# Optimization experiments

Hardware: AMD Instinct MI355X
Metric: run time of the kernel (lower is better)

The kernel has to match this reference:

```python
import jax, jax.numpy as jnp
import numpy as np
import math

NUM_HEADS = 16
HEAD_DIM = 64


def _apply_rope(x, sin2, cos2):
    # x: [B,H,S,D]; sin2/cos2: [1,1,S,D] interleaved-duplicated sin/cos
    x_even = x[..., ::2]
    x_odd = x[..., 1::2]
    rot = jnp.stack([-x_odd, x_even], axis=-1).reshape(x.shape)
    return x * cos2 + rot * sin2


def setup_inputs() -> dict:
    key = jax.random.key(0)
    k1, k2, k3, k4 = jax.random.split(key, 4)
    B, S, D = 2, 2048, 1024
    hidden_states = jax.random.normal(k1, (B, S, D), dtype=jnp.float32)
    # RoFormer-style sinusoidal_pos: first half sin, second half cos
    half = HEAD_DIM // 2
    inv_freq = 1.0 / (10000.0 ** (np.arange(0, half, dtype=np.float32) / half))
    t = np.arange(S, dtype=np.float32)
    ang = np.einsum('s,d->sd', t, inv_freq)  # [S, half]
    sinusoidal_pos = jnp.asarray(
        np.concatenate([np.sin(ang), np.cos(ang)], axis=-1)[None, None]
    )  # [1,1,S,HEAD_DIM]
    attention_mask = jnp.zeros((B, 1, 1, S), dtype=jnp.float32)
    scale = 0.02
    Wq = jax.random.normal(k2, (D, D), dtype=jnp.float32) * scale
    Wk = jax.random.normal(k3, (D, D), dtype=jnp.float32) * scale
    Wv = jax.random.normal(k4, (D, D), dtype=jnp.float32) * scale
    return {
        'hidden_states': hidden_states,
        'sinusoidal_pos': sinusoidal_pos,
        'attention_mask': attention_mask,
        'Wq': Wq,
        'Wk': Wk,
        'Wv': Wv,
    }


def reference(hidden_states, sinusoidal_pos, attention_mask, Wq, Wk, Wv):
    B, S, D = hidden_states.shape
    H, Dh = NUM_HEADS, HEAD_DIM

    def split_heads(x):  # [B,S,D] -> [B,H,S,Dh]
        return x.reshape(B, S, H, Dh).transpose(0, 2, 1, 3)

    q = split_heads(hidden_states @ Wq.T)
    k = split_heads(hidden_states @ Wk.T)
    v = split_heads(hidden_states @ Wv.T)

    # sinusoidal_pos: [1,1,S,Dh]; chunk -> sin, cos halves, then interleave-duplicate
    sin, cos = jnp.split(sinusoidal_pos, 2, axis=-1)
    sin2 = jnp.repeat(sin, 2, axis=-1)
    cos2 = jnp.repeat(cos, 2, axis=-1)
    q = _apply_rope(q, sin2, cos2)
    k = _apply_rope(k, sin2, cos2)

    scores = jnp.einsum('bhqd,bhkd->bhqk', q, k) / math.sqrt(Dh)
    scores = scores + attention_mask  # additive mask broadcasts over heads/query
    probs = jax.nn.softmax(scores, axis=-1)
    ctx = jnp.einsum('bhqk,bhkd->bhqd', probs, v)
    ctx = ctx.transpose(0, 2, 1, 3).reshape(B, S, D)
    return ctx
```

## Files before the change

kernel.cpp:

```cpp
#include <hip/hip_runtime.h>
#include <math.h>

#define B_  2
#define S_  2048
#define D_  1024
#define H_  16
#define DH  64
#define M_  (B_*S_)
#define QKSZ 4194304

typedef __attribute__((ext_vector_type(4)))  float  f32x4;
typedef __attribute__((ext_vector_type(16))) float  f32x16;
typedef __attribute__((ext_vector_type(8)))  short  short8;
typedef __attribute__((ext_vector_type(8)))  unsigned short ushort8;
typedef __attribute__((ext_vector_type(4)))  unsigned short us4;

static __device__ __forceinline__ unsigned short f2bf(float x) {
    union { float f; unsigned int u; } v; v.f = x;
    unsigned int u = v.u;
    u += 0x7fffu + ((u >> 16) & 1u);
    return (unsigned short)(u >> 16);
}

typedef __attribute__((address_space(3))) void       lds_void;
typedef const __attribute__((address_space(1))) void gbl_void;

static __device__ __forceinline__ void gload_lds16(const unsigned short* g,
                                                   unsigned short* l) {
    __builtin_amdgcn_global_load_lds((gbl_void*)g, (lds_void*)l, 16, 0, 0);
}

__global__ __launch_bounds__(256) void cvt_all(
    const float* __restrict__ hid, const float* __restrict__ Wq,
    const float* __restrict__ Wk,  const float* __restrict__ Wv,
    unsigned short* __restrict__ hb, unsigned short* __restrict__ wb)
{
    const size_t i = ((size_t)blockIdx.x * 256 + threadIdx.x) * 8;
    const float* s; unsigned short* d;
    if (i < 4194304) { s = hid + i; d = hb + i; }
    else {
        size_t j = i - 4194304;
        const float* w = (j < 1048576) ? Wq : (j < 2097152) ? Wk : Wv;
        s = w + (j & 1048575);
        d = wb + j;
    }
    float4 a = *(const float4*)s, b = *(const float4*)(s + 4);
    ushort8 o;
    o[0] = f2bf(a.x); o[1] = f2bf(a.y); o[2] = f2bf(a.z); o[3] = f2bf(a.w);
    o[4] = f2bf(b.x); o[5] = f2bf(b.y); o[6] = f2bf(b.z); o[7] = f2bf(b.w);
    *(ushort8*)d = o;
}

__global__ __launch_bounds__(256) void qkv_gemm(
    const unsigned short* __restrict__ hb,
    const unsigned short* __restrict__ wb,
    const float* __restrict__ sp,
    unsigned short* __restrict__ qk_ws,
    unsigned short* __restrict__ vt_ws)
{
    __shared__ unsigned short As[128 * 32];
    __shared__ unsigned short Bs[128 * 32];

    const int tid    = threadIdx.x;
    const int tile_m = (blockIdx.x & 31) * 128;
    const int tile_n = (blockIdx.x >> 5) * 128;

    const int w  = tid >> 6, lane = tid & 63;
    const int wr = w >> 1,  wc = w & 1;
    const int g  = lane >> 4, c16 = lane & 15;
    const int lr = lane >> 2;
    const int lc = (lane & 3) * 8;

    const size_t arow = (size_t)(tile_m + w * 16 + lr) * 1024 + lc;
    const size_t brow = (size_t)(tile_n + w * 16 + lr) * 1024 + lc;
    unsigned short* lA0 = &As[(w * 16) * 32];
    unsigned short* lA1 = &As[(w * 16 + 64) * 32];
    unsigned short* lB0 = &Bs[(w * 16) * 32];
    unsigned short* lB1 = &Bs[(w * 16 + 64) * 32];

    f32x4 acc[4][4];
    #pragma unroll
    for (int i = 0; i < 4; ++i)
        #pragma unroll
        for (int j = 0; j < 4; ++j)
            acc[i][j][0] = acc[i][j][1] = acc[i][j][2] = acc[i][j][3] = 0.f;

    for (int k0 = 0; k0 < 1024; k0 += 32) {
        gload_lds16(hb + arow + k0,             lA0);
        gload_lds16(hb + arow + 64 * 1024 + k0, lA1);
        gload_lds16(wb + brow + k0,             lB0);
        gload_lds16(wb + brow + 64 * 1024 + k0, lB1);
        __syncthreads();

        short8 af[4], bf[4];
        #pragma unroll
        for (int i = 0; i < 4; ++i)
            af[i] = *(const short8*)&As[(wr * 64 + i * 16 + c16) * 32 + g * 8];
        #pragma unroll
        for (int j = 0; j < 4; ++j)
            bf[j] = *(const short8*)&Bs[(wc * 64 + j * 16 + c16) * 32 + g * 8];
        __builtin_amdgcn_s_setprio(1);
        #pragma unroll
        for (int i = 0; i < 4; ++i)
            #pragma unroll
            for (int j = 0; j < 4; ++j)
                acc[i][j] = __builtin_amdgcn_mfma_f32_16x16x32_bf16(
                    af[i], bf[j], acc[i][j], 0, 0, 0);
        __builtin_amdgcn_s_setprio(0);
        __syncthreads();
    }

    if (tile_n < 2048) {
        const int isK = (tile_n >= 1024) ? 1 : 0;
        unsigned short* qkb = qk_ws + (size_t)isK * QKSZ;
        const int head = ((tile_n - (isK ? 1024 : 0)) + wc * 64) >> 6;
        #pragma unroll
        for (int j = 0; j < 4; ++j) {
            const int dh = j * 16 + c16;
            const int p  = dh >> 1;
            const int odd = dh & 1;
            #pragma unroll
            for (int i = 0; i < 4; ++i) {
                #pragma unroll
                for (int r = 0; r < 4; ++r) {
                    const int m = tile_m + wr * 64 + i * 16 + 4 * g + r;
                    const int b = m >> 11, s = m & 2047;
                    float v    = acc[i][j][r];
                    float part = __shfl_xor(v, 1);
                    float sv = sp[s * 64 + p];
                    float cv = sp[s * 64 + 32 + p];
                    float o  = odd ? (v * cv + part * sv) : (v * cv - part * sv);
                    qkb[((size_t)(b * H_ + head) * S_ + s) * DH + dh] = f2bf(o);
                }
            }
        }
    } else {
        const int head = (tile_n - 2048 + wc * 64) >> 6;
        #pragma unroll
        for (int j = 0; j < 4; ++j) {
            const int dh = j * 16 + c16;
            #pragma unroll
            for (int i = 0; i < 4; ++i) {
                const int m0 = tile_m + wr * 64 + i * 16 + 4 * g;
                const int b = m0 >> 11, s0 = m0 & 2047;
                us4 o;
                o[0] = f2bf(acc[i][j][0]); o[1] = f2bf(acc[i][j][1]);
                o[2] = f2bf(acc[i][j][2]); o[3] = f2bf(acc[i][j][3]);
                *(us4*)&vt_ws[((size_t)(b * H_ + head) * DH + dh) * S_ + s0] = o;
            }
        }
    }
}

__global__ __launch_bounds__(256) void qkv_proj(
    const float* __restrict__ hid,
    const float* __restrict__ sp,
    const float* __restrict__ Wq,
    const float* __restrict__ Wk,
    const float* __restrict__ Wv,
    unsigned short* __restrict__ qk_ws,
    unsigned short* __restrict__ vt_ws)
{
    __shared__ unsigned short As[128 * 32];
    __shared__ unsigned short Bs[128 * 32];

    const int tid    = threadIdx.x;
    const int tile_m = (blockIdx.x & 31) * 128;
    const int tile_n = (blockIdx.x >> 5) * 128;

    const float* W; int nloc;
    if (tile_n < 1024)      { W = Wq; nloc = tile_n; }
    else if (tile_n < 2048) { W = Wk; nloc = tile_n - 1024; }
    else                    { W = Wv; nloc = tile_n - 2048; }

    const int w    = tid >> 6, lane = tid & 63;
    const int wr   = w >> 1,  wc   = w & 1;
    const int g    = lane >> 4, c16 = lane & 15;
    const int srow = tid >> 3;
    const int scol = (tid & 7) * 4;

    f32x4 acc[4][4];
    #pragma unroll
    for (int i = 0; i < 4; ++i)
        #pragma unroll
        for (int j = 0; j < 4; ++j)
            acc[i][j][0] = acc[i][j][1] = acc[i][j][2] = acc[i][j][3] = 0.f;

    for (int k0 = 0; k0 < 1024; k0 += 32) {
        #pragma unroll
        for (int p = 0; p < 4; ++p) {
            const int row = p * 32 + srow;
            float4 a = *(const float4*)&hid[(size_t)(tile_m + row) * 1024 + k0 + scol];
            float4 b = *(const float4*)&W  [(size_t)(nloc   + row) * 1024 + k0 + scol];
            us4 ap, bp;
            ap[0] = f2bf(a.x); ap[1] = f2bf(a.y); ap[2] = f2bf(a.z); ap[3] = f2bf(a.w);
            bp[0] = f2bf(b.x); bp[1] = f2bf(b.y); bp[2] = f2bf(b.z); bp[3] = f2bf(b.w);
            *(us4*)&As[p * 1024 + tid * 4] = ap;
            *(us4*)&Bs[p * 1024 + tid * 4] = bp;
        }
        __syncthreads();

        short8 af[4], bf[4];
        #pragma unroll
        for (int i = 0; i < 4; ++i)
            af[i] = *(const short8*)&As[(wr * 64 + i * 16 + c16) * 32 + g * 8];
        #pragma unroll
        for (int j = 0; j < 4; ++j)
            bf[j] = *(const short8*)&Bs[(wc * 64 + j * 16 + c16) * 32 + g * 8];
        #pragma unroll
        for (int i = 0; i < 4; ++i)
            #pragma unroll
            for (int j = 0; j < 4; ++j)
                acc[i][j] = __builtin_amdgcn_mfma_f32_16x16x32_bf16(
                    af[i], bf[j], acc[i][j], 0, 0, 0);
        __syncthreads();
    }

    if (tile_n < 2048) {
        const int isK = (tile_n >= 1024) ? 1 : 0;
        unsigned short* qkb = qk_ws + (size_t)isK * QKSZ;
        const int head = ((tile_n - (isK ? 1024 : 0)) + wc * 64) >> 6;
        #pragma unroll
        for (int j = 0; j < 4; ++j) {
            const int dh = j * 16 + c16;
            const int p  = dh >> 1;
            const int odd = dh & 1;
            #pragma unroll
            for (int i = 0; i < 4; ++i) {
                #pragma unroll
                for (int r = 0; r < 4; ++r) {
                    const int m = tile_m + wr * 64 + i * 16 + 4 * g + r;
                    const int b = m >> 11, s = m & 2047;
                    float v    = acc[i][j][r];
                    float part = __shfl_xor(v, 1);
                    float sv = sp[s * 64 + p];
                    float cv = sp[s * 64 + 32 + p];
                    float o  = odd ? (v * cv + part * sv) : (v * cv - part * sv);
                    qkb[((size_t)(b * H_ + head) * S_ + s) * DH + dh] = f2bf(o);
                }
            }
        }
    } else {
        const int head = (tile_n - 2048 + wc * 64) >> 6;
        #pragma unroll
        for (int j = 0; j < 4; ++j) {
            const int dh = j * 16 + c16;
            #pragma unroll
            for (int i = 0; i < 4; ++i) {
                const int m0 = tile_m + wr * 64 + i * 16 + 4 * g;
                const int b = m0 >> 11, s0 = m0 & 2047;
                us4 o;
                o[0] = f2bf(acc[i][j][0]); o[1] = f2bf(acc[i][j][1]);
                o[2] = f2bf(acc[i][j][2]); o[3] = f2bf(acc[i][j][3]);
                *(us4*)&vt_ws[((size_t)(b * H_ + head) * DH + dh) * S_ + s0] = o;
            }
        }
    }
}

__global__ __launch_bounds__(256, 2) void attn_fwd(
    const unsigned short* __restrict__ qk_ws,
    const unsigned short* __restrict__ vt_ws,
    const float* __restrict__ maskp,
    float* __restrict__ out)
{
    __shared__ unsigned short K_lds[2][64 * 64];
    __shared__ unsigned short V_lds[2][64 * 64];

    const int tid  = threadIdx.x;
    const int w    = tid >> 6, lane = tid & 63;
    const int hi   = lane >> 5, c32 = lane & 31;
    const int qt   = blockIdx.x & 15;
    const int bh   = blockIdx.x >> 4;
    const int b    = bh >> 4, h = bh & 15;

    const unsigned short* qp = qk_ws + (size_t)bh * (S_ * DH);
    const unsigned short* kp = qk_ws + QKSZ + (size_t)bh * (S_ * DH);
    const unsigned short* vp = vt_ws + (size_t)bh * (DH * S_);
    const float* mp = maskp + b * S_;

    const int q = qt * 128 + w * 32 + c32;

    short8 qf[4];
    #pragma unroll
    for (int ks = 0; ks < 4; ++ks)
        qf[ks] = *(const short8*)&qp[(size_t)q * DH + ks * 16 + 8 * hi];

    f32x16 ctx[2];
    #pragma unroll
    for (int d = 0; d < 2; ++d)
        #pragma unroll
        for (int r = 0; r < 16; ++r) ctx[d][r] = 0.f;
    float mrow = -1e30f, lsum = 0.f;

    ushort8 rk[2], rv[2];
    const int su0 = tid, su1 = tid + 256;

    auto LOADT = [&](int t) {
        const int kv = t * 64;
        {
            int row = su0 >> 3, c = (su0 & 7) * 8;
            rk[0] = *(const ushort8*)&kp[(size_t)(kv + row) * DH + c];
            rv[0] = *(const ushort8*)&vp[(size_t)row * S_ + kv + c];
        }
        {
            int row = su1 >> 3, c = (su1 & 7) * 8;
            rk[1] = *(const ushort8*)&kp[(size_t)(kv + row) * DH + c];
            rv[1] = *(const ushort8*)&vp[(size_t)row * S_ + kv + c];
        }
    };
    auto WRITET = [&](int buf) {
        {
            int row = su0 >> 3, c = (su0 & 7) * 16;
            int off = (row * 128 + c) ^ ((row & 7) << 4);
            *(ushort8*)((char*)&K_lds[buf][0] + off) = rk[0];
            *(ushort8*)((char*)&V_lds[buf][0] + off) = rv[0];
        }
        {
            int row = su1 >> 3, c = (su1 & 7) * 16;
            int off = (row * 128 + c) ^ ((row & 7) << 4);
            *(ushort8*)((char*)&K_lds[buf][0] + off) = rk[1];
            *(ushort8*)((char*)&V_lds[buf][0] + off) = rv[1];
        }
    };

    LOADT(0); WRITET(0); LOADT(1);
    __syncthreads();

    const int NT = S_ / 64;
    for (int t = 0; t < NT; ++t) {
        const int cur = t & 1;
        const int kv  = t * 64;
        const char* Kb = (const char*)&K_lds[cur][0];
        const char* Vb = (const char*)&V_lds[cur][0];

        f32x16 sa0, sa1;
        #pragma unroll
        for (int r = 0; r < 16; ++r) { sa0[r] = 0.f; sa1[r] = 0.f; }
        __builtin_amdgcn_s_setprio(1);
        #pragma unroll
        for (int ks = 0; ks < 4; ++ks) {
            const int colb = ks * 32 + hi * 16;
            short8 kf0 = *(const short8*)(Kb + ((c32 * 128 + colb) ^ ((c32 & 7) << 4)));
            short8 kf1 = *(const short8*)(Kb + (((32 + c32) * 128 + colb) ^ ((c32 & 7) << 4)));
            sa0 = __builtin_amdgcn_mfma_f32_32x32x16_bf16(kf0, qf[ks], sa0, 0, 0, 0);
            sa1 = __builtin_amdgcn_mfma_f32_32x32x16_bf16(kf1, qf[ks], sa1, 0, 0, 0);
        }
        __builtin_amdgcn_s_setprio(0);

        float sc0[16], sc1[16];
        #pragma unroll
        for (int r = 0; r < 16; ++r) {
            const int koff = (r & 3) + 8 * (r >> 2) + 4 * hi;
            sc0[r] = sa0[r] * 0.125f + mp[kv + koff];
            sc1[r] = sa1[r] * 0.125f + mp[kv + 32 + koff];
        }

        float pm = sc0[0];
        #pragma unroll
        for (int r = 1; r < 16; ++r) pm = fmaxf(pm, sc0[r]);
        #pragma unroll
        for (int r = 0; r < 16; ++r) pm = fmaxf(pm, sc1[r]);
        pm = fmaxf(pm, __shfl_xor(pm, 32));

        if (!__all(pm - mrow <= 8.0f)) {
            const float mnew = fmaxf(mrow, pm);
            const float fac  = __expf(mrow - mnew);
            mrow = mnew;
            lsum *= fac;
            #pragma unroll
            for (int d = 0; d < 2; ++d)
                #pragma unroll
                for (int r = 0; r < 16; ++r) ctx[d][r] *= fac;
        }

        float p0[16], p1[16];
        float ps = 0.f;
        #pragma unroll
        for (int r = 0; r < 16; ++r) { p0[r] = __expf(sc0[r] - mrow); ps += p0[r]; }
        #pragma unroll
        for (int r = 0; r < 16; ++r) { p1[r] = __expf(sc1[r] - mrow); ps += p1[r]; }
        lsum += ps;

        short8 pf[4];
        #pragma unroll
        for (int ks4 = 0; ks4 < 4; ++ks4) {
            const float* pp = (ks4 < 2) ? p0 : p1;
            const int k8 = (ks4 & 1) * 8;
            unsigned int a0 = ((unsigned int)f2bf(pp[k8 + 1]) << 16) | f2bf(pp[k8 + 0]);
            unsigned int a1 = ((unsigned int)f2bf(pp[k8 + 3]) << 16) | f2bf(pp[k8 + 2]);
            unsigned int b0 = ((unsigned int)f2bf(pp[k8 + 5]) << 16) | f2bf(pp[k8 + 4]);
            unsigned int b1 = ((unsigned int)f2bf(pp[k8 + 7]) << 16) | f2bf(pp[k8 + 6]);
            unsigned int ax0 = (unsigned int)__shfl_xor((int)a0, 32);
            unsigned int ax1 = (unsigned int)__shfl_xor((int)a1, 32);
            unsigned int bx0 = (unsigned int)__shfl_xor((int)b0, 32);
            unsigned int bx1 = (unsigned int)__shfl_xor((int)b1, 32);
            union { unsigned int u[4]; short8 v; } fr;
            fr.u[0] = hi ? bx0 : a0;
            fr.u[1] = hi ? bx1 : a1;
            fr.u[2] = hi ? b0  : ax0;
            fr.u[3] = hi ? b1  : ax1;
            pf[ks4] = fr.v;
        }

        if (t + 1 < NT) {
            __syncthreads();
            WRITET(cur ^ 1);
            if (t + 2 < NT) LOADT(t + 2);
        }

        __builtin_amdgcn_s_setprio(1);
        #pragma unroll
        for (int ks4 = 0; ks4 < 4; ++ks4) {
            const int colb = ks4 * 32 + hi * 16;
            short8 vf0 = *(const short8*)(Vb + ((c32 * 128 + colb) ^ ((c32 & 7) << 4)));
            short8 vf1 = *(const short8*)(Vb + (((32 + c32) * 128 + colb) ^ ((c32 & 7) << 4)));
            ctx[0] = __builtin_amdgcn_mfma_f32_32x32x16_bf16(vf0, pf[ks4], ctx[0], 0, 0, 0);
            ctx[1] = __builtin_amdgcn_mfma_f32_32x32x16_bf16(vf1, pf[ks4], ctx[1], 0, 0, 0);
        }
        __builtin_amdgcn_s_setprio(0);

        if (t + 1 < NT) __syncthreads();
    }

    const float inv = 1.0f / (lsum + __shfl_xor(lsum, 32));

    float* ob = out + ((size_t)(b * S_ + q) * D_) + h * DH;
    #pragma unroll
    for (int d = 0; d < 2; ++d)
        #pragma unroll
        for (int q4 = 0; q4 < 4; ++q4) {
            f32x4 st;
            st[0] = ctx[d][q4 * 4 + 0] * inv;
            st[1] = ctx[d][q4 * 4 + 1] * inv;
            st[2] = ctx[d][q4 * 4 + 2] * inv;
            st[3] = ctx[d][q4 * 4 + 3] * inv;
            *(f32x4*)&ob[d * 32 + 8 * q4 + 4 * hi] = st;
        }
}

extern "C" void kernel_launch(void* const* d_in, const int* in_sizes, int n_in,
                              void* d_out, int out_size, void* d_ws, size_t ws_size,
                              hipStream_t stream) {
    (void)in_sizes; (void)n_in; (void)out_size;
    const float* hid  = (const float*)d_in[0];
    const float* sp   = (const float*)d_in[1];
    const float* mask = (const float*)d_in[2];
    const float* Wq   = (const float*)d_in[3];
    const float* Wk   = (const float*)d_in[4];
    const float* Wv   = (const float*)d_in[5];
    float* out = (float*)d_out;

    unsigned short* qk_ws = (unsigned short*)d_ws;
    unsigned short* vt_ws = qk_ws + 2 * (size_t)QKSZ;
    unsigned short* hb    = vt_ws + (size_t)QKSZ;
    unsigned short* wb    = hb + 4194304;

    const size_t NEED = 39845888;
    if (ws_size >= NEED) {
        cvt_all<<<dim3(3584), dim3(256), 0, stream>>>(hid, Wq, Wk, Wv, hb, wb);
        qkv_gemm<<<dim3(32 * 24), dim3(256), 0, stream>>>(hb, wb, sp, qk_ws, vt_ws);
    } else {
        qkv_proj<<<dim3(32 * 24), dim3(256), 0, stream>>>(hid, sp, Wq, Wk, Wv, qk_ws, vt_ws);
    }
    attn_fwd<<<dim3(32 * 16), dim3(256), 0, stream>>>(qk_ws, vt_ws, mask, out);
}
```

Baseline: 197.2 us.

## Widen GEMM K-tile with swizzled LDS, fold softmax scale into Q, use exp2

The QKV GEMM now stages a 64-wide K slice per iteration into XOR-swizzled LDS, which halves the barrier count and is meant to cut LDS bank conflicts. The attention kernel pre-scales Q by log2(e)/sqrt(d) in the GEMM epilogue and uses raw v_exp_f32 (exp2), which drops the per-score multiply. It also caches the mask in LDS pre-multiplied by log2(e), uses packed bf16 conversion for P, and changes the rescale threshold and max reduction. The risks are higher LDS use, which may lower occupancy, and small numerical differences from scaling Q before bf16 rounding.

```diff
diff --git a/kernel.cpp b/kernel.cpp
--- a/kernel.cpp
+++ b/kernel.cpp
@@ -1,4 +1,5 @@
 #include <hip/hip_runtime.h>
+#include <hip/hip_bf16.h>
 #include <math.h>
 
 #define B_  2
@@ -6,7 +7,6 @@
 #define D_  1024
 #define H_  16
 #define DH  64
-#define M_  (B_*S_)
 #define QKSZ 4194304
 
 typedef __attribute__((ext_vector_type(4)))  float  f32x4;
@@ -15,11 +15,26 @@
 typedef __attribute__((ext_vector_type(8)))  unsigned short ushort8;
 typedef __attribute__((ext_vector_type(4)))  unsigned short us4;
 
+#define LOG2E 1.44269504f
+#define QSCL  0.18033688f
+
 static __device__ __forceinline__ unsigned short f2bf(float x) {
     union { float f; unsigned int u; } v; v.f = x;
     unsigned int u = v.u;
     u += 0x7fffu + ((u >> 16) & 1u);
     return (unsigned short)(u >> 16);
+}
+
+static __device__ __forceinline__ unsigned int pk2(float lo, float hi) {
+    union { __hip_bfloat162 b; unsigned int u; } c;
+    c.b = __float22bfloat162_rn(float2{lo, hi});
+    return c.u;
+}
+
+static __device__ __forceinline__ float exp2a(float x) {
+    float r;
+    asm("v_exp_f32 %0, %1" : "=v"(r) : "v"(x));
+    return r;
 }
 
 typedef __attribute__((address_space(3))) void       lds_void;
@@ -58,8 +73,8 @@
     unsigned short* __restrict__ qk_ws,
     unsigned short* __restrict__ vt_ws)
 {
-    __shared__ unsigned short As[128 * 32];
-    __shared__ unsigned short Bs[128 * 32];
+    __shared__ unsigned short As[128 * 64];
+    __shared__ unsigned short Bs[128 * 64];
 
     const int tid    = threadIdx.x;
     const int tile_m = (blockIdx.x & 31) * 128;
@@ -68,15 +83,11 @@
     const int w  = tid >> 6, lane = tid & 63;
     const int wr = w >> 1,  wc = w & 1;
     const int g  = lane >> 4, c16 = lane & 15;
-    const int lr = lane >> 2;
-    const int lc = (lane & 3) * 8;
-
-    const size_t arow = (size_t)(tile_m + w * 16 + lr) * 1024 + lc;
-    const size_t brow = (size_t)(tile_n + w * 16 + lr) * 1024 + lc;
-    unsigned short* lA0 = &As[(w * 16) * 32];
-    unsigned short* lA1 = &As[(w * 16 + 64) * 32];
-    unsigned short* lB0 = &Bs[(w * 16) * 32];
-    unsigned short* lB1 = &Bs[(w * 16 + 64) * 32];
+
+    const int rg = lane >> 3;
+    const int cg = (lane & 7) ^ rg;
+    const size_t a_base = (size_t)(tile_m + w * 8 + rg) * 1024 + cg * 8;
+    const size_t b_base = (size_t)(tile_n + w * 8 + rg) * 1024 + cg * 8;
 
     f32x4 acc[4][4];
     #pragma unroll
@@ -85,33 +96,42 @@
         for (int j = 0; j < 4; ++j)
             acc[i][j][0] = acc[i][j][1] = acc[i][j][2] = acc[i][j][3] = 0.f;
 
-    for (int k0 = 0; k0 < 1024; k0 += 32) {
-        gload_lds16(hb + arow + k0,             lA0);
-        gload_lds16(hb + arow + 64 * 1024 + k0, lA1);
-        gload_lds16(wb + brow + k0,             lB0);
-        gload_lds16(wb + brow + 64 * 1024 + k0, lB1);
+    for (int k0 = 0; k0 < 1024; k0 += 64) {
+        #pragma unroll
+        for (int p = 0; p < 4; ++p) {
+            gload_lds16(hb + a_base + (size_t)p * 32768 + k0, &As[(p * 32 + w * 8) * 64]);
+            gload_lds16(wb + b_base + (size_t)p * 32768 + k0, &Bs[(p * 32 + w * 8) * 64]);
+        }
         __syncthreads();
 
-        short8 af[4], bf[4];
-        #pragma unroll
-        for (int i = 0; i < 4; ++i)
-            af[i] = *(const short8*)&As[(wr * 64 + i * 16 + c16) * 32 + g * 8];
-        #pragma unroll
-        for (int j = 0; j < 4; ++j)
-            bf[j] = *(const short8*)&Bs[(wc * 64 + j * 16 + c16) * 32 + g * 8];
-        __builtin_amdgcn_s_setprio(1);
-        #pragma unroll
-        for (int i = 0; i < 4; ++i)
-            #pragma unroll
-            for (int j = 0; j < 4; ++j)
-                acc[i][j] = __builtin_amdgcn_mfma_f32_16x16x32_bf16(
-                    af[i], bf[j], acc[i][j], 0, 0, 0);
-        __builtin_amdgcn_s_setprio(0);
+        #pragma unroll
+        for (int kk = 0; kk < 2; ++kk) {
+            short8 af[4], bf[4];
+            #pragma unroll
+            for (int i = 0; i < 4; ++i) {
+                const int row = wr * 64 + i * 16 + c16;
+                af[i] = *(const short8*)&As[row * 64 + (((kk << 2) + g) ^ (row & 7)) * 8];
+            }
+            #pragma unroll
+            for (int j = 0; j < 4; ++j) {
+                const int row = wc * 64 + j * 16 + c16;
+                bf[j] = *(const short8*)&Bs[row * 64 + (((kk << 2) + g) ^ (row & 7)) * 8];
+            }
+            __builtin_amdgcn_s_setprio(1);
+            #pragma unroll
+            for (int i = 0; i < 4; ++i)
+                #pragma unroll
+                for (int j = 0; j < 4; ++j)
+                    acc[i][j] = __builtin_amdgcn_mfma_f32_16x16x32_bf16(
+                        af[i], bf[j], acc[i][j], 0, 0, 0);
+            __builtin_amdgcn_s_setprio(0);
+        }
         __syncthreads();
     }
 
     if (tile_n < 2048) {
         const int isK = (tile_n >= 1024) ? 1 : 0;
+        const float qscl = isK ? 1.0f : QSCL;
         unsigned short* qkb = qk_ws + (size_t)isK * QKSZ;
         const int head = ((tile_n - (isK ? 1024 : 0)) + wc * 64) >> 6;
         #pragma unroll
@@ -129,7 +149,7 @@
                     float part = __shfl_xor(v, 1);
                     float sv = sp[s * 64 + p];
                     float cv = sp[s * 64 + 32 + p];
-                    float o  = odd ? (v * cv + part * sv) : (v * cv - part * sv);
+                    float o  = (odd ? (v * cv + part * sv) : (v * cv - part * sv)) * qscl;
                     qkb[((size_t)(b * H_ + head) * S_ + s) * DH + dh] = f2bf(o);
                 }
             }
@@ -150,6 +170,198 @@
             }
         }
     }
+}
+
+__global__ __launch_bounds__(256, 2) void attn_fwd(
+    const unsigned short* __restrict__ qk_ws,
+    const unsigned short* __restrict__ vt_ws,
+    const float* __restrict__ maskp,
+    float* __restrict__ out)
+{
+    __shared__ unsigned short K_lds[2][64 * 64];
+    __shared__ unsigned short V_lds[2][64 * 64];
+    __shared__ float M_lds[2048];
+
+    const int tid  = threadIdx.x;
+    const int w    = tid >> 6, lane = tid & 63;
+    const int hi   = lane >> 5, c32 = lane & 31;
+    const int qt   = blockIdx.x & 15;
+    const int bh   = blockIdx.x >> 4;
+    const int b    = bh >> 4, h = bh & 15;
+
+    const unsigned short* qp = qk_ws + (size_t)bh * (S_ * DH);
+    const unsigned short* kp = qk_ws + QKSZ + (size_t)bh * (S_ * DH);
+    const unsigned short* vp = vt_ws + (size_t)bh * (DH * S_);
+    const float* mp = maskp + b * S_;
+
+    const int q = qt * 128 + w * 32 + c32;
+
+    short8 qf[4];
+    #pragma unroll
+    for (int ks = 0; ks < 4; ++ks)
+        qf[ks] = *(const short8*)&qp[(size_t)q * DH + ks * 16 + 8 * hi];
+
+    f32x16 ctx[2];
+    #pragma unroll
+    for (int d = 0; d < 2; ++d)
+        #pragma unroll
+        for (int r = 0; r < 16; ++r) ctx[d][r] = 0.f;
+    float mrow = -1e30f, lsum = 0.f;
+
+    ushort8 rk[2], rv[2];
+    const int su0 = tid, su1 = tid + 256;
+
+    auto LOADT = [&](int t) {
+        const int kv = t * 64;
+        {
+            int row = su0 >> 3, c = (su0 & 7) * 8;
+            rk[0] = *(const ushort8*)&kp[(size_t)(kv + row) * DH + c];
+            rv[0] = *(const ushort8*)&vp[(size_t)row * S_ + kv + c];
+        }
+        {
+            int row = su1 >> 3, c = (su1 & 7) * 8;
+            rk[1] = *(const ushort8*)&kp[(size_t)(kv + row) * DH + c];
+            rv[1] = *(const ushort8*)&vp[(size_t)row * S_ + kv + c];
+        }
+    };
+    auto WRITET = [&](int buf) {
+        {
+            int row = su0 >> 3, c = (su0 & 7) * 16;
+            int off = (row * 128 + c) ^ ((row & 7) << 4);
+            *(ushort8*)((char*)&K_lds[buf][0] + off) = rk[0];
+            *(ushort8*)((char*)&V_lds[buf][0] + off) = rv[0];
+        }
+        {
+            int row = su1 >> 3, c = (su1 & 7) * 16;
+            int off = (row * 128 + c) ^ ((row & 7) << 4);
+            *(ushort8*)((char*)&K_lds[buf][0] + off) = rk[1];
+            *(ushort8*)((char*)&V_lds[buf][0] + off) = rv[1];
+        }
+    };
+
+    LOADT(0); WRITET(0); LOADT(1);
+    {
+        float4 ma = *(const float4*)&mp[tid * 8];
+        float4 mb2 = *(const float4*)&mp[tid * 8 + 4];
+        M_lds[tid * 8 + 0] = ma.x * LOG2E;  M_lds[tid * 8 + 1] = ma.y * LOG2E;
+        M_lds[tid * 8 + 2] = ma.z * LOG2E;  M_lds[tid * 8 + 3] = ma.w * LOG2E;
+        M_lds[tid * 8 + 4] = mb2.x * LOG2E; M_lds[tid * 8 + 5] = mb2.y * LOG2E;
+        M_lds[tid * 8 + 6] = mb2.z * LOG2E; M_lds[tid * 8 + 7] = mb2.w * LOG2E;
+    }
+    __syncthreads();
+
+    const int NT = S_ / 64;
+    for (int t = 0; t < NT; ++t) {
+        const int cur = t & 1;
+        const int kv  = t * 64;
+        const char* Kb = (const char*)&K_lds[cur][0];
+        const char* Vb = (const char*)&V_lds[cur][0];
+
+        f32x16 sa0, sa1;
+        #pragma unroll
+        for (int r = 0; r < 16; ++r) { sa0[r] = 0.f; sa1[r] = 0.f; }
+        __builtin_amdgcn_s_setprio(1);
+        #pragma unroll
+        for (int ks = 0; ks < 4; ++ks) {
+            const int colb = ks * 32 + hi * 16;
+            short8 kf0 = *(const short8*)(Kb + ((c32 * 128 + colb) ^ ((c32 & 7) << 4)));
+            short8 kf1 = *(const short8*)(Kb + (((32 + c32) * 128 + colb) ^ ((c32 & 7) << 4)));
+            sa0 = __builtin_amdgcn_mfma_f32_32x32x16_bf16(kf0, qf[ks], sa0, 0, 0, 0);
+            sa1 = __builtin_amdgcn_mfma_f32_32x32x16_bf16(kf1, qf[ks], sa1, 0, 0, 0);
+        }
+        __builtin_amdgcn_s_setprio(0);
+
+        float sc0[16], sc1[16];
+        #pragma unroll
+        for (int r = 0; r < 16; ++r) {
+            const int koff = (r & 3) + 8 * (r >> 2) + 4 * hi;
+            sc0[r] = sa0[r] + M_lds[kv + koff];
+            sc1[r] = sa1[r] + M_lds[kv + 32 + koff];
+        }
+
+        float tm[8];
+        #pragma unroll
+        for (int r2 = 0; r2 < 8; ++r2)
+            tm[r2] = fmaxf(fmaxf(sc0[r2 * 2], sc0[r2 * 2 + 1]),
+                           fmaxf(sc1[r2 * 2], sc1[r2 * 2 + 1]));
+        float pm = fmaxf(fmaxf(fmaxf(tm[0], tm[1]), fmaxf(tm[2], tm[3])),
+                         fmaxf(fmaxf(tm[4], tm[5]), fmaxf(tm[6], tm[7])));
+        pm = fmaxf(pm, __shfl_xor(pm, 32));
+
+        if (!__all(pm - mrow <= 11.54f)) {
+            const float mnew = fmaxf(mrow, pm);
+            const float fac  = exp2a(mrow - mnew);
+            mrow = mnew;
+            lsum *= fac;
+            #pragma unroll
+            for (int d = 0; d < 2; ++d)
+                #pragma unroll
+                for (int r = 0; r < 16; ++r) ctx[d][r] *= fac;
+        }
+
+        float p0[16], p1[16];
+        float ps = 0.f;
+        #pragma unroll
+        for (int r = 0; r < 16; ++r) { p0[r] = exp2a(sc0[r] - mrow); ps += p0[r]; }
+        #pragma unroll
+        for (int r = 0; r < 16; ++r) { p1[r] = exp2a(sc1[r] - mrow); ps += p1[r]; }
+        lsum += ps;
+
+        short8 pf[4];
+        #pragma unroll
+        for (int ks4 = 0; ks4 < 4; ++ks4) {
+            const float* pp = (ks4 < 2) ? p0 : p1;
+            const int k8 = (ks4 & 1) * 8;
+            unsigned int a0 = pk2(pp[k8 + 0], pp[k8 + 1]);
+            unsigned int a1 = pk2(pp[k8 + 2], pp[k8 + 3]);
+            unsigned int b0 = pk2(pp[k8 + 4], pp[k8 + 5]);
+            unsigned int b1 = pk2(pp[k8 + 6], pp[k8 + 7]);
+            unsigned int ax0 = (unsigned int)__shfl_xor((int)a0, 32);
+            unsigned int ax1 = (unsigned int)__shfl_xor((int)a1, 32);
+            unsigned int bx0 = (unsigned int)__shfl_xor((int)b0, 32);
+            unsigned int bx1 = (unsigned int)__shfl_xor((int)b1, 32);
+            union { unsigned int u[4]; short8 v; } fr;
+            fr.u[0] = hi ? bx0 : a0;
+            fr.u[1] = hi ? bx1 : a1;
+            fr.u[2] = hi ? b0  : ax0;
+            fr.u[3] = hi ? b1  : ax1;
+            pf[ks4] = fr.v;
+        }
+
+        if (t + 1 < NT) {
+            __syncthreads();
+            WRITET(cur ^ 1);
+            if (t + 2 < NT) LOADT(t + 2);
+        }
+
+        __builtin_amdgcn_s_setprio(1);
+        #pragma unroll
+        for (int ks4 = 0; ks4 < 4; ++ks4) {
+            const int colb = ks4 * 32 + hi * 16;
+            short8 vf0 = *(const short8*)(Vb + ((c32 * 128 + colb) ^ ((c32 & 7) << 4)));
+            short8 vf1 = *(const short8*)(Vb + (((32 + c32) * 128 + colb) ^ ((c32 & 7) << 4)));
+            ctx[0] = __builtin_amdgcn_mfma_f32_32x32x16_bf16(vf0, pf[ks4], ctx[0], 0, 0, 0);
+            ctx[1] = __builtin_amdgcn_mfma_f32_32x32x16_bf16(vf1, pf[ks4], ctx[1], 0, 0, 0);
+        }
+        __builtin_amdgcn_s_setprio(0);
+
+        if (t + 1 < NT) __syncthreads();
+    }
+
+    const float inv = 1.0f / (lsum + __shfl_xor(lsum, 32));
+
+    float* ob = out + ((size_t)(b * S_ + q) * D_) + h * DH;
+    #pragma unroll
+    for (int d = 0; d < 2; ++d)
+        #pragma unroll
+        for (int q4 = 0; q4 < 4; ++q4) {
+            f32x4 st;
+            st[0] = ctx[d][q4 * 4 + 0] * inv;
+            st[1] = ctx[d][q4 * 4 + 1] * inv;
+            st[2] = ctx[d][q4 * 4 + 2] * inv;
+            st[3] = ctx[d][q4 * 4 + 3] * inv;
+            *(f32x4*)&ob[d * 32 + 8 * q4 + 4 * hi] = st;
+        }
 }
 
 __global__ __launch_bounds__(256) void qkv_proj(
@@ -218,6 +430,7 @@
 
     if (tile_n < 2048) {
         const int isK = (tile_n >= 1024) ? 1 : 0;
+        const float qscl = isK ? 1.0f : QSCL;
         unsigned short* qkb = qk_ws + (size_t)isK * QKSZ;
         const int head = ((tile_n - (isK ? 1024 : 0)) + wc * 64) >> 6;
         #pragma unroll
@@ -235,7 +448,7 @@
                     float part = __shfl_xor(v, 1);
                     float sv = sp[s * 64 + p];
                     float cv = sp[s * 64 + 32 + p];
-                    float o  = odd ? (v * cv + part * sv) : (v * cv - part * sv);
+                    float o  = (odd ? (v * cv + part * sv) : (v * cv - part * sv)) * qscl;
                     qkb[((size_t)(b * H_ + head) * S_ + s) * DH + dh] = f2bf(o);
                 }
             }
@@ -256,187 +469,6 @@
             }
         }
     }
-}
-
-__global__ __launch_bounds__(256, 2) void attn_fwd(
-    const unsigned short* __restrict__ qk_ws,
-    const unsigned short* __restrict__ vt_ws,
-    const float* __restrict__ maskp,
-    float* __restrict__ out)
-{
-    __shared__ unsigned short K_lds[2][64 * 64];
-    __shared__ unsigned short V_lds[2][64 * 64];
-
-    const int tid  = threadIdx.x;
-    const int w    = tid >> 6, lane = tid & 63;
-    const int hi   = lane >> 5, c32 = lane & 31;
-    const int qt   = blockIdx.x & 15;
-    const int bh   = blockIdx.x >> 4;
-    const int b    = bh >> 4, h = bh & 15;
-
-    const unsigned short* qp = qk_ws + (size_t)bh * (S_ * DH);
-    const unsigned short* kp = qk_ws + QKSZ + (size_t)bh * (S_ * DH);
-    const unsigned short* vp = vt_ws + (size_t)bh * (DH * S_);
-    const float* mp = maskp + b * S_;
-
-    const int q = qt * 128 + w * 32 + c32;
-
-    short8 qf[4];
-    #pragma unroll
-    for (int ks = 0; ks < 4; ++ks)
-        qf[ks] = *(const short8*)&qp[(size_t)q * DH + ks * 16 + 8 * hi];
-
-    f32x16 ctx[2];
-    #pragma unroll
-    for (int d = 0; d < 2; ++d)
-        #pragma unroll
-        for (int r = 0; r < 16; ++r) ctx[d][r] = 0.f;
-    float mrow = -1e30f, lsum = 0.f;
-
-    ushort8 rk[2], rv[2];
-    const int su0 = tid, su1 = tid + 256;
-
-    auto LOADT = [&](int t) {
-        const int kv = t * 64;
-        {
-            int row = su0 >> 3, c = (su0 & 7) * 8;
-            rk[0] = *(const ushort8*)&kp[(size_t)(kv + row) * DH + c];
-            rv[0] = *(const ushort8*)&vp[(size_t)row * S_ + kv + c];
-        }
-        {
-            int row = su1 >> 3, c = (su1 & 7) * 8;
-            rk[1] = *(const ushort8*)&kp[(size_t)(kv + row) * DH + c];
-            rv[1] = *(const ushort8*)&vp[(size_t)row * S_ + kv + c];
-        }
-    };
-    auto WRITET = [&](int buf) {
-        {
-            int row = su0 >> 3, c = (su0 & 7) * 16;
-            int off = (row * 128 + c) ^ ((row & 7) << 4);
-            *(ushort8*)((char*)&K_lds[buf][0] + off) = rk[0];
-            *(ushort8*)((char*)&V_lds[buf][0] + off) = rv[0];
-        }
-        {
-            int row = su1 >> 3, c = (su1 & 7) * 16;
-            int off = (row * 128 + c) ^ ((row & 7) << 4);
-            *(ushort8*)((char*)&K_lds[buf][0] + off) = rk[1];
-            *(ushort8*)((char*)&V_lds[buf][0] + off) = rv[1];
-        }
-    };
-
-    LOADT(0); WRITET(0); LOADT(1);
-    __syncthreads();
-
-    const int NT = S_ / 64;
-    for (int t = 0; t < NT; ++t) {
-        const int cur = t & 1;
-        const int kv  = t * 64;
-        const char* Kb = (const char*)&K_lds[cur][0];
-        const char* Vb = (const char*)&V_lds[cur][0];
-
-        f32x16 sa0, sa1;
-        #pragma unroll
-        for (int r = 0; r < 16; ++r) { sa0[r] = 0.f; sa1[r] = 0.f; }
-        __builtin_amdgcn_s_setprio(1);
-        #pragma unroll
-        for (int ks = 0; ks < 4; ++ks) {
-            const int colb = ks * 32 + hi * 16;
-            short8 kf0 = *(const short8*)(Kb + ((c32 * 128 + colb) ^ ((c32 & 7) << 4)));
-            short8 kf1 = *(const short8*)(Kb + (((32 + c32) * 128 + colb) ^ ((c32 & 7) << 4)));
-            sa0 = __builtin_amdgcn_mfma_f32_32x32x16_bf16(kf0, qf[ks], sa0, 0, 0, 0);
-            sa1 = __builtin_amdgcn_mfma_f32_32x32x16_bf16(kf1, qf[ks], sa1, 0, 0, 0);
-        }
-        __builtin_amdgcn_s_setprio(0);
-
-        float sc0[16], sc1[16];
-        #pragma unroll
-        for (int r = 0; r < 16; ++r) {
-            const int koff = (r & 3) + 8 * (r >> 2) + 4 * hi;
-            sc0[r] = sa0[r] * 0.125f + mp[kv + koff];
-            sc1[r] = sa1[r] * 0.125f + mp[kv + 32 + koff];
-        }
-
-        float pm = sc0[0];
-        #pragma unroll
-        for (int r = 1; r < 16; ++r) pm = fmaxf(pm, sc0[r]);
-        #pragma unroll
-        for (int r = 0; r < 16; ++r) pm = fmaxf(pm, sc1[r]);
-        pm = fmaxf(pm, __shfl_xor(pm, 32));
-
-        if (!__all(pm - mrow <= 8.0f)) {
-            const float mnew = fmaxf(mrow, pm);
-            const float fac  = __expf(mrow - mnew);
-            mrow = mnew;
-            lsum *= fac;
-            #pragma unroll
-            for (int d = 0; d < 2; ++d)
-                #pragma unroll
-                for (int r = 0; r < 16; ++r) ctx[d][r] *= fac;
-        }
-
-        float p0[16], p1[16];
-        float ps = 0.f;
-        #pragma unroll
-        for (int r = 0; r < 16; ++r) { p0[r] = __expf(sc0[r] - mrow); ps += p0[r]; }
-        #pragma unroll
-        for (int r = 0; r < 16; ++r) { p1[r] = __expf(sc1[r] - mrow); ps += p1[r]; }
-        lsum += ps;
-
-        short8 pf[4];
-        #pragma unroll
-        for (int ks4 = 0; ks4 < 4; ++ks4) {
-            const float* pp = (ks4 < 2) ? p0 : p1;
-            const int k8 = (ks4 & 1) * 8;
-            unsigned int a0 = ((unsigned int)f2bf(pp[k8 + 1]) << 16) | f2bf(pp[k8 + 0]);
-            unsigned int a1 = ((unsigned int)f2bf(pp[k8 + 3]) << 16) | f2bf(pp[k8 + 2]);
-            unsigned int b0 = ((unsigned int)f2bf(pp[k8 + 5]) << 16) | f2bf(pp[k8 + 4]);
-            unsigned int b1 = ((unsigned int)f2bf(pp[k8 + 7]) << 16) | f2bf(pp[k8 + 6]);
-            unsigned int ax0 = (unsigned int)__shfl_xor((int)a0, 32);
-            unsigned int ax1 = (unsigned int)__shfl_xor((int)a1, 32);
-            unsigned int bx0 = (unsigned int)__shfl_xor((int)b0, 32);
-            unsigned int bx1 = (unsigned int)__shfl_xor((int)b1, 32);
-            union { unsigned int u[4]; short8 v; } fr;
-            fr.u[0] = hi ? bx0 : a0;
-            fr.u[1] = hi ? bx1 : a1;
-            fr.u[2] = hi ? b0  : ax0;
-            fr.u[3] = hi ? b1  : ax1;
-            pf[ks4] = fr.v;
-        }
-
-        if (t + 1 < NT) {
-            __syncthreads();
-            WRITET(cur ^ 1);
-            if (t + 2 < NT) LOADT(t + 2);
-        }
-
-        __builtin_amdgcn_s_setprio(1);
-        #pragma unroll
-        for (int ks4 = 0; ks4 < 4; ++ks4) {
-            const int colb = ks4 * 32 + hi * 16;
-            short8 vf0 = *(const short8*)(Vb + ((c32 * 128 + colb) ^ ((c32 & 7) << 4)));
-            short8 vf1 = *(const short8*)(Vb + (((32 + c32) * 128 + colb) ^ ((c32 & 7) << 4)));
-            ctx[0] = __builtin_amdgcn_mfma_f32_32x32x16_bf16(vf0, pf[ks4], ctx[0], 0, 0, 0);
-            ctx[1] = __builtin_amdgcn_mfma_f32_32x32x16_bf16(vf1, pf[ks4], ctx[1], 0, 0, 0);
-        }
-        __builtin_amdgcn_s_setprio(0);
-
-        if (t + 1 < NT) __syncthreads();
-    }
-
-    const float inv = 1.0f / (lsum + __shfl_xor(lsum, 32));
-
-    float* ob = out + ((size_t)(b * S_ + q) * D_) + h * DH;
-    #pragma unroll
-    for (int d = 0; d < 2; ++d)
-        #pragma unroll
-        for (int q4 = 0; q4 < 4; ++q4) {
-            f32x4 st;
-            st[0] = ctx[d][q4 * 4 + 0] * inv;
-            st[1] = ctx[d][q4 * 4 + 1] * inv;
-            st[2] = ctx[d][q4 * 4 + 2] * inv;
-            st[3] = ctx[d][q4 * 4 + 3] * inv;
-            *(f32x4*)&ob[d * 32 + 8 * q4 + 4 * hi] = st;
-        }
 }
 
 extern "C" void kernel_launch(void* const* d_in, const int* in_sizes, int n_in,
```

Result: faster. 185.8 us (-5.8%).
